# Optimization experiments

Measured on AMD Instinct MI355X. Metric: run time of the kernel, lower is better.

Reference implementation:

```python
import jax, jax.numpy as jnp
import numpy as np

N_NODES = 100000
N_EDGES = 1600000


def _add_self_loops(edge_index, num_nodes):
    loop = jnp.arange(num_nodes, dtype=edge_index.dtype)
    src = jnp.concatenate([edge_index[0], loop])
    dst = jnp.concatenate([edge_index[1], loop])
    return src, dst


def _gcn_conv(x, src, dst, W, b, num_nodes):
    # PyG GCNConv: h = x W, then symmetric-normalized scatter-add aggregation.
    h = x @ W  # [N, F_out]
    ones = jnp.ones(src.shape[0], dtype=x.dtype)
    deg = jax.ops.segment_sum(ones, dst, num_segments=num_nodes)  # in-degree incl. self-loops
    dinv = jnp.where(deg > 0, jax.lax.rsqrt(deg), 0.0)
    norm = dinv[src] * dinv[dst]  # [E]
    msg = h[src] * norm[:, None]  # irregular gather, [E, F_out]
    out = jax.ops.segment_sum(msg, dst, num_segments=num_nodes)  # scatter-add, [N, F_out]
    return out + b


def setup_inputs() -> dict:
    key = jax.random.key(0)
    ks = jax.random.split(key, 4)
    x = jax.random.uniform(ks[0], (N_NODES, 32), dtype=jnp.float32)
    edge_index = jax.random.randint(ks[1], (2, N_EDGES), 0, N_NODES, dtype=jnp.int64)
    W1 = jax.random.normal(ks[2], (32, 64), dtype=jnp.float32) * (1.0 / np.sqrt(32))
    b1 = jnp.zeros((64,), dtype=jnp.float32)
    W2 = jax.random.normal(ks[3], (64, 128), dtype=jnp.float32) * (1.0 / np.sqrt(64))
    b2 = jnp.zeros((128,), dtype=jnp.float32)
    return {"x": x, "edge_index": edge_index, "W1": W1, "b1": b1, "W2": W2, "b2": b2}


def reference(x, edge_index, W1, b1, W2, b2):
    num_nodes = x.shape[0]
    src, dst = _add_self_loops(edge_index, num_nodes)
    h = _gcn_conv(x, src, dst, W1, b1, num_nodes)
    h = jax.nn.relu(h)
    out = _gcn_conv(h, src, dst, W2, b2, num_nodes)
    return out
```

## Files before the change

### kernel.cpp

```cpp
#include <hip/hip_runtime.h>
#include <hip/hip_fp16.h>

static inline int cdiv(int a, int b) { return (a + b - 1) / b; }

#define BK_SHIFT 8
#define NBLK2 1024
#define SCAN_BS 1024
#define MAXB 6144

struct h2x4 { __half2 a, b, c, d; };

__global__ __launch_bounds__(256) void kb1(const int* __restrict__ dst, int E, int epb, int nbuk,
                                           int* __restrict__ cnt) {
    __shared__ int h[512];
    int blk = blockIdx.x;
    for (int b = threadIdx.x; b < nbuk; b += 256) h[b] = 0;
    __syncthreads();
    int beg = blk * epb, end = min(E, beg + epb);
    for (int e = beg + threadIdx.x; e < end; e += 256)
        atomicAdd(&h[dst[e] >> BK_SHIFT], 1);
    __syncthreads();
    for (int b = threadIdx.x; b < nbuk; b += 256) cnt[(size_t)b * NBLK2 + blk] = h[b];
}

__global__ __launch_bounds__(SCAN_BS) void k_blocksum(const int* __restrict__ v, int n, int* __restrict__ bsum) {
    __shared__ int s[SCAN_BS];
    int t = threadIdx.x;
    int i = blockIdx.x * SCAN_BS + t;
    s[t] = (i < n) ? v[i] : 0;
    __syncthreads();
    for (int off = SCAN_BS / 2; off > 0; off >>= 1) {
        if (t < off) s[t] += s[t + off];
        __syncthreads();
    }
    if (t == 0) bsum[blockIdx.x] = s[0];
}

__global__ __launch_bounds__(512) void k_scan_bsums(const int* __restrict__ bsum, int NB, int* __restrict__ boff) {
    __shared__ int s[512];
    int t = threadIdx.x;
    int v = (t < NB) ? bsum[t] : 0;
    s[t] = v;
    __syncthreads();
    for (int off = 1; off < 512; off <<= 1) {
        int u = (t >= off) ? s[t - off] : 0;
        __syncthreads();
        s[t] += u;
        __syncthreads();
    }
    if (t < NB) boff[t] = s[t] - v;
}

__global__ __launch_bounds__(SCAN_BS) void k_scan_final(const int* __restrict__ v, int n,
                                                        const int* __restrict__ boff,
                                                        int* __restrict__ outp, int E) {
    __shared__ int s[SCAN_BS];
    int t = threadIdx.x;
    int i = blockIdx.x * SCAN_BS + t;
    int x = (i < n) ? v[i] : 0;
    s[t] = x;
    __syncthreads();
    for (int off = 1; off < SCAN_BS; off <<= 1) {
        int u = (t >= off) ? s[t - off] : 0;
        __syncthreads();
        s[t] += u;
        __syncthreads();
    }
    if (i < n) outp[i] = boff[blockIdx.x] + s[t] - x;
    if (blockIdx.x == 0 && t == 0) outp[n] = E;
}

__global__ __launch_bounds__(256) void kb2(const int* __restrict__ ei, int E, int epb, int nbuk,
                                           const int* __restrict__ cbase,
                                           unsigned int* __restrict__ pairs) {
    __shared__ int lb[512];
    int blk = blockIdx.x;
    for (int b = threadIdx.x; b < nbuk; b += 256) lb[b] = cbase[(size_t)b * NBLK2 + blk];
    __syncthreads();
    int beg = blk * epb, end = min(E, beg + epb);
    const int* dst = ei + E;
    for (int e = beg + threadIdx.x; e < end; e += 256) {
        int d = dst[e];
        int s = ei[e];
        int slot = atomicAdd(&lb[d >> BK_SHIFT], 1);
        pairs[slot] = (unsigned)s | ((unsigned)(d & 255) << 17);
    }
}

__global__ __launch_bounds__(1024) void k_sortbucket(const unsigned int* __restrict__ pairs,
                                                     const int* __restrict__ cbase, int nbuk, int N, int E,
                                                     int* __restrict__ csr_src,
                                                     int* __restrict__ offsets,
                                                     float* __restrict__ dinv) {
    __shared__ int c[256];
    __shared__ int ex[256];
    __shared__ int sorted[MAXB];
    int b = blockIdx.x;
    int tid = threadIdx.x;
    int base = cbase[(size_t)b * NBLK2];
    int endp = cbase[(size_t)(b + 1) * NBLK2];
    int n = endp - base;
    if (tid < 256) c[tid] = 0;
    __syncthreads();
    int sr_[6], dl_[6], rk_[6];
#pragma unroll
    for (int k = 0; k < 6; ++k) {
        int i = tid + k * 1024;
        if (i < n) {
            unsigned int p = pairs[base + i];
            sr_[k] = (int)(p & 0x1FFFFu);
            dl_[k] = (int)(p >> 17);
            rk_[k] = atomicAdd(&c[dl_[k]], 1);
        }
    }
    __syncthreads();
    if (tid < 256) ex[tid] = c[tid];
    __syncthreads();
    for (int off = 1; off < 256; off <<= 1) {
        int u = (tid >= off && tid < 256) ? ex[tid - off] : 0;
        __syncthreads();
        if (tid < 256) ex[tid] += u;
        __syncthreads();
    }
    if (tid < 256) ex[tid] -= c[tid];
    __syncthreads();
#pragma unroll
    for (int k = 0; k < 6; ++k) {
        int i = tid + k * 1024;
        if (i < n) sorted[ex[dl_[k]] + rk_[k]] = sr_[k];
    }
    __syncthreads();
    for (int i = tid; i < n; i += 1024) csr_src[base + i] = sorted[i];
    if (tid < 256) {
        int g = (b << BK_SHIFT) + tid;
        if (g < N) {
            offsets[g] = base + ex[tid];
            dinv[g] = rsqrtf((float)(c[tid] + 1));
        }
    }
    if (b == 0 && tid == 0) offsets[N] = E;
}

__global__ __launch_bounds__(256) void k_cast32(const float* __restrict__ x, const float* __restrict__ dinv,
                                                __half* __restrict__ xh, int N) {
    int i = blockIdx.x * 256 + threadIdx.x;
    if (i >= N * 8) return;
    int g = i >> 3;
    float di = dinv[g];
    float4 v = ((const float4*)x)[i];
    __half2 h0 = __floats2half2_rn(v.x * di, v.y * di);
    __half2 h1 = __floats2half2_rn(v.z * di, v.w * di);
    ((__half2*)xh)[2 * i] = h0;
    ((__half2*)xh)[2 * i + 1] = h1;
}

template <int F>
__global__ __launch_bounds__(256) void k_agg(const __half* __restrict__ feat,
                                             const int* __restrict__ offsets,
                                             const int* __restrict__ csr_src,
                                             const float* __restrict__ dinv,
                                             float* __restrict__ out, int N) {
    constexpr int L = F / 8;
    int t = blockIdx.x * 256 + threadIdx.x;
    int g = t / L;
    int q = t % L;
    if (g >= N) return;
    const h2x4* f8 = (const h2x4*)feat;
    int beg = offsets[g];
    int end = offsets[g + 1];
    float di = dinv[g];
    float acc[8];
    {
        h2x4 w = f8[(size_t)g * L + q];
        float2 p0 = __half22float2(w.a), p1 = __half22float2(w.b);
        float2 p2 = __half22float2(w.c), p3 = __half22float2(w.d);
        acc[0] = p0.x; acc[1] = p0.y; acc[2] = p1.x; acc[3] = p1.y;
        acc[4] = p2.x; acc[5] = p2.y; acc[6] = p3.x; acc[7] = p3.y;
    }
    int e = beg;
    for (; e + 4 <= end; e += 4) {
        int s0 = csr_src[e + 0], s1 = csr_src[e + 1], s2 = csr_src[e + 2], s3 = csr_src[e + 3];
        h2x4 w0 = f8[(size_t)s0 * L + q];
        h2x4 w1 = f8[(size_t)s1 * L + q];
        h2x4 w2 = f8[(size_t)s2 * L + q];
        h2x4 w3 = f8[(size_t)s3 * L + q];
        float2 u;
        u = __half22float2(w0.a); acc[0] += u.x; acc[1] += u.y;
        u = __half22float2(w0.b); acc[2] += u.x; acc[3] += u.y;
        u = __half22float2(w0.c); acc[4] += u.x; acc[5] += u.y;
        u = __half22float2(w0.d); acc[6] += u.x; acc[7] += u.y;
        u = __half22float2(w1.a); acc[0] += u.x; acc[1] += u.y;
        u = __half22float2(w1.b); acc[2] += u.x; acc[3] += u.y;
        u = __half22float2(w1.c); acc[4] += u.x; acc[5] += u.y;
        u = __half22float2(w1.d); acc[6] += u.x; acc[7] += u.y;
        u = __half22float2(w2.a); acc[0] += u.x; acc[1] += u.y;
        u = __half22float2(w2.b); acc[2] += u.x; acc[3] += u.y;
        u = __half22float2(w2.c); acc[4] += u.x; acc[5] += u.y;
        u = __half22float2(w2.d); acc[6] += u.x; acc[7] += u.y;
        u = __half22float2(w3.a); acc[0] += u.x; acc[1] += u.y;
        u = __half22float2(w3.b); acc[2] += u.x; acc[3] += u.y;
        u = __half22float2(w3.c); acc[4] += u.x; acc[5] += u.y;
        u = __half22float2(w3.d); acc[6] += u.x; acc[7] += u.y;
    }
    for (; e < end; ++e) {
        h2x4 w = f8[(size_t)csr_src[e] * L + q];
        float2 u;
        u = __half22float2(w.a); acc[0] += u.x; acc[1] += u.y;
        u = __half22float2(w.b); acc[2] += u.x; acc[3] += u.y;
        u = __half22float2(w.c); acc[4] += u.x; acc[5] += u.y;
        u = __half22float2(w.d); acc[6] += u.x; acc[7] += u.y;
    }
    float4 o0 = make_float4(acc[0] * di, acc[1] * di, acc[2] * di, acc[3] * di);
    float4 o1 = make_float4(acc[4] * di, acc[5] * di, acc[6] * di, acc[7] * di);
    ((float4*)out)[(size_t)g * (F / 4) + q * 2] = o0;
    ((float4*)out)[(size_t)g * (F / 4) + q * 2 + 1] = o1;
}

__global__ __launch_bounds__(256) void k_gemm1(const float* __restrict__ A, const float* __restrict__ W,
                                               const float* __restrict__ b, const float* __restrict__ dinv,
                                               __half* __restrict__ out, int N) {
    __shared__ float sA[32][68];
    __shared__ float sW[32][64];
    int tid = threadIdx.x;
    int row0 = blockIdx.x * 64;

    {
        const float4* Wv = (const float4*)W;
        float4* sWv = (float4*)&sW[0][0];
        sWv[tid] = Wv[tid];
        sWv[tid + 256] = Wv[tid + 256];
    }
    {
        int row = tid >> 2;
        int gr = row0 + row;
        int kq = (tid & 3) * 4;
#pragma unroll
        for (int i = 0; i < 2; ++i) {
            int k0 = kq + 16 * i;
            float4 v = (gr < N) ? *(const float4*)(A + (size_t)gr * 32 + k0)
                                : make_float4(0.f, 0.f, 0.f, 0.f);
            sA[k0 + 0][row] = v.x;
            sA[k0 + 1][row] = v.y;
            sA[k0 + 2][row] = v.z;
            sA[k0 + 3][row] = v.w;
        }
    }
    __syncthreads();

    int tm = tid & 15, tn = tid >> 4;
    float acc[4][4];
#pragma unroll
    for (int i = 0; i < 4; ++i) {
        float4 bb = *(const float4*)(b + tn * 4);
        acc[i][0] = bb.x; acc[i][1] = bb.y; acc[i][2] = bb.z; acc[i][3] = bb.w;
    }
#pragma unroll 4
    for (int k = 0; k < 32; ++k) {
        float4 a = *(const float4*)&sA[k][tm * 4];
        float4 w = *(const float4*)&sW[k][tn * 4];
        float av[4] = {a.x, a.y, a.z, a.w};
        float wv[4] = {w.x, w.y, w.z, w.w};
#pragma unroll
        for (int i = 0; i < 4; ++i)
#pragma unroll
            for (int j = 0; j < 4; ++j) acc[i][j] = fmaf(av[i], wv[j], acc[i][j]);
    }
#pragma unroll
    for (int i = 0; i < 4; ++i) {
        int row = row0 + tm * 4 + i;
        if (row < N) {
            float di = dinv[row];
            __half2 p0 = __floats2half2_rn(fmaxf(acc[i][0], 0.f) * di, fmaxf(acc[i][1], 0.f) * di);
            __half2 p1 = __floats2half2_rn(fmaxf(acc[i][2], 0.f) * di, fmaxf(acc[i][3], 0.f) * di);
            __half2* op = (__half2*)(out + (size_t)row * 64);
            op[tn * 2] = p0;
            op[tn * 2 + 1] = p1;
        }
    }
}

__global__ __launch_bounds__(256) void k_gemm2(const float* __restrict__ A, const float* __restrict__ W,
                                               const float* __restrict__ b, float* __restrict__ out, int N) {
    __shared__ float sA[64][68];
    __shared__ float sW[64][128];
    int tid = threadIdx.x;
    int row0 = blockIdx.x * 64;

    {
        const float4* Wv = (const float4*)W;
        float4* sWv = (float4*)&sW[0][0];
#pragma unroll
        for (int i = 0; i < 8; ++i) sWv[tid + 256 * i] = Wv[tid + 256 * i];
    }
    {
        int row = tid >> 2;
        int gr = row0 + row;
        int kq = (tid & 3) * 4;
#pragma unroll
        for (int i = 0; i < 4; ++i) {
            int k0 = kq + 16 * i;
            float4 v = (gr < N) ? *(const float4*)(A + (size_t)gr * 64 + k0)
                                : make_float4(0.f, 0.f, 0.f, 0.f);
            sA[k0 + 0][row] = v.x;
            sA[k0 + 1][row] = v.y;
            sA[k0 + 2][row] = v.z;
            sA[k0 + 3][row] = v.w;
        }
    }
    __syncthreads();

    int tm = tid & 15, tn = tid >> 4;
    float acc[4][8];
    {
        float4 b0 = *(const float4*)(b + tn * 8);
        float4 b1 = *(const float4*)(b + tn * 8 + 4);
#pragma unroll
        for (int i = 0; i < 4; ++i) {
            acc[i][0] = b0.x; acc[i][1] = b0.y; acc[i][2] = b0.z; acc[i][3] = b0.w;
            acc[i][4] = b1.x; acc[i][5] = b1.y; acc[i][6] = b1.z; acc[i][7] = b1.w;
        }
    }
#pragma unroll 4
    for (int k = 0; k < 64; ++k) {
        float4 a = *(const float4*)&sA[k][tm * 4];
        float4 w0 = *(const float4*)&sW[k][tn * 8];
        float4 w1 = *(const float4*)&sW[k][tn * 8 + 4];
        float av[4] = {a.x, a.y, a.z, a.w};
        float wv[8] = {w0.x, w0.y, w0.z, w0.w, w1.x, w1.y, w1.z, w1.w};
#pragma unroll
        for (int i = 0; i < 4; ++i)
#pragma unroll
            for (int j = 0; j < 8; ++j) acc[i][j] = fmaf(av[i], wv[j], acc[i][j]);
    }
#pragma unroll
    for (int i = 0; i < 4; ++i) {
        int row = row0 + tm * 4 + i;
        if (row < N) {
            *(float4*)(out + (size_t)row * 128 + tn * 8) =
                make_float4(acc[i][0], acc[i][1], acc[i][2], acc[i][3]);
            *(float4*)(out + (size_t)row * 128 + tn * 8 + 4) =
                make_float4(acc[i][4], acc[i][5], acc[i][6], acc[i][7]);
        }
    }
}

extern "C" void kernel_launch(void* const* d_in, const int* in_sizes, int n_in,
                              void* d_out, int out_size, void* d_ws, size_t ws_size,
                              hipStream_t stream) {
    const float* x  = (const float*)d_in[0];
    const int*   ei = (const int*)d_in[1];
    const float* W1 = (const float*)d_in[2];
    const float* b1 = (const float*)d_in[3];
    const float* W2 = (const float*)d_in[4];
    const float* b2 = (const float*)d_in[5];
    float* out = (float*)d_out;

    const int N = in_sizes[0] / 32;
    const int E = in_sizes[1] / 2;
    const int epb = cdiv(E, NBLK2);
    const int nbuk = cdiv(N, 1 << BK_SHIFT);
    const int clen = nbuk * NBLK2;

    char* ws = (char*)d_ws;
    size_t off = 0;
    auto walloc = [&](size_t bytes) -> void* {
        void* p = ws + off;
        off = (off + bytes + 255) & ~(size_t)255;
        return p;
    };
    int*          cnt     = (int*)          walloc((size_t)(clen + 4) * 4);
    int*          cbase   = (int*)          walloc((size_t)(clen + 4) * 4);
    int*          bsum    = (int*)          walloc(512 * 4);
    int*          boff    = (int*)          walloc(512 * 4);
    unsigned int* pairs   = (unsigned int*) walloc((size_t)E * 4);
    int*          csr_src = (int*)          walloc((size_t)E * 4);
    int*          offsets = (int*)          walloc((size_t)(N + 4) * 4);
    float*        dinv    = (float*)        walloc((size_t)N * 4);
    __half*       xh      = (__half*)       walloc((size_t)N * 32 * 2);
    float*        a1      = (float*)        walloc((size_t)N * 32 * 4);
    __half*       h2h     = (__half*)       walloc((size_t)N * 64 * 2);
    float*        a2      = (float*)        walloc((size_t)N * 64 * 4);
    (void)ws_size; (void)n_in; (void)out_size;

    kb1<<<NBLK2, 256, 0, stream>>>(ei + E, E, epb, nbuk, cnt);

    const int NB = cdiv(clen, SCAN_BS);
    k_blocksum<<<NB, SCAN_BS, 0, stream>>>(cnt, clen, bsum);
    k_scan_bsums<<<1, 512, 0, stream>>>(bsum, NB, boff);
    k_scan_final<<<NB, SCAN_BS, 0, stream>>>(cnt, clen, boff, cbase, E);

    kb2<<<NBLK2, 256, 0, stream>>>(ei, E, epb, nbuk, cbase, pairs);
    k_sortbucket<<<nbuk, 1024, 0, stream>>>(pairs, cbase, nbuk, N, E, csr_src, offsets, dinv);

    k_cast32<<<cdiv(N * 8, 256), 256, 0, stream>>>(x, dinv, xh, N);

    k_agg<32><<<cdiv(N * 4, 256), 256, 0, stream>>>(xh, offsets, csr_src, dinv, a1, N);
    k_gemm1<<<cdiv(N, 64), 256, 0, stream>>>(a1, W1, b1, dinv, h2h, N);

    k_agg<64><<<cdiv(N * 8, 256), 256, 0, stream>>>(h2h, offsets, csr_src, dinv, a2, N);
    k_gemm2<<<cdiv(N, 64), 256, 0, stream>>>(a2, W2, b2, out, N);
}
```

Before: 151.6 us.

## Fuse sparse aggregation with dense GEMM in both GCN layers

Merges each aggregation kernel with the following small GEMM. The aggregated rows now stay in shared memory instead of being written to and re-read from fp32 global buffers a1/a2, and two launches are removed. The second layer's tile shrinks to 32 rows, so each block reloads the full 32KB W2 more often. The gather phase and the GEMM phase also can no longer overlap across separate kernels.

```diff
diff --git a/kernel.cpp b/kernel.cpp
--- a/kernel.cpp
+++ b/kernel.cpp
@@ -154,75 +154,18 @@
     ((__half2*)xh)[2 * i + 1] = h1;
 }
 
-template <int F>
-__global__ __launch_bounds__(256) void k_agg(const __half* __restrict__ feat,
-                                             const int* __restrict__ offsets,
-                                             const int* __restrict__ csr_src,
-                                             const float* __restrict__ dinv,
-                                             float* __restrict__ out, int N) {
-    constexpr int L = F / 8;
-    int t = blockIdx.x * 256 + threadIdx.x;
-    int g = t / L;
-    int q = t % L;
-    if (g >= N) return;
-    const h2x4* f8 = (const h2x4*)feat;
-    int beg = offsets[g];
-    int end = offsets[g + 1];
-    float di = dinv[g];
-    float acc[8];
-    {
-        h2x4 w = f8[(size_t)g * L + q];
-        float2 p0 = __half22float2(w.a), p1 = __half22float2(w.b);
-        float2 p2 = __half22float2(w.c), p3 = __half22float2(w.d);
-        acc[0] = p0.x; acc[1] = p0.y; acc[2] = p1.x; acc[3] = p1.y;
-        acc[4] = p2.x; acc[5] = p2.y; acc[6] = p3.x; acc[7] = p3.y;
-    }
-    int e = beg;
-    for (; e + 4 <= end; e += 4) {
-        int s0 = csr_src[e + 0], s1 = csr_src[e + 1], s2 = csr_src[e + 2], s3 = csr_src[e + 3];
-        h2x4 w0 = f8[(size_t)s0 * L + q];
-        h2x4 w1 = f8[(size_t)s1 * L + q];
-        h2x4 w2 = f8[(size_t)s2 * L + q];
-        h2x4 w3 = f8[(size_t)s3 * L + q];
-        float2 u;
-        u = __half22float2(w0.a); acc[0] += u.x; acc[1] += u.y;
-        u = __half22float2(w0.b); acc[2] += u.x; acc[3] += u.y;
-        u = __half22float2(w0.c); acc[4] += u.x; acc[5] += u.y;
-        u = __half22float2(w0.d); acc[6] += u.x; acc[7] += u.y;
-        u = __half22float2(w1.a); acc[0] += u.x; acc[1] += u.y;
-        u = __half22float2(w1.b); acc[2] += u.x; acc[3] += u.y;
-        u = __half22float2(w1.c); acc[4] += u.x; acc[5] += u.y;
-        u = __half22float2(w1.d); acc[6] += u.x; acc[7] += u.y;
-        u = __half22float2(w2.a); acc[0] += u.x; acc[1] += u.y;
-        u = __half22float2(w2.b); acc[2] += u.x; acc[3] += u.y;
-        u = __half22float2(w2.c); acc[4] += u.x; acc[5] += u.y;
-        u = __half22float2(w2.d); acc[6] += u.x; acc[7] += u.y;
-        u = __half22float2(w3.a); acc[0] += u.x; acc[1] += u.y;
-        u = __half22float2(w3.b); acc[2] += u.x; acc[3] += u.y;
-        u = __half22float2(w3.c); acc[4] += u.x; acc[5] += u.y;
-        u = __half22float2(w3.d); acc[6] += u.x; acc[7] += u.y;
-    }
-    for (; e < end; ++e) {
-        h2x4 w = f8[(size_t)csr_src[e] * L + q];
-        float2 u;
-        u = __half22float2(w.a); acc[0] += u.x; acc[1] += u.y;
-        u = __half22float2(w.b); acc[2] += u.x; acc[3] += u.y;
-        u = __half22float2(w.c); acc[4] += u.x; acc[5] += u.y;
-        u = __half22float2(w.d); acc[6] += u.x; acc[7] += u.y;
-    }
-    float4 o0 = make_float4(acc[0] * di, acc[1] * di, acc[2] * di, acc[3] * di);
-    float4 o1 = make_float4(acc[4] * di, acc[5] * di, acc[6] * di, acc[7] * di);
-    ((float4*)out)[(size_t)g * (F / 4) + q * 2] = o0;
-    ((float4*)out)[(size_t)g * (F / 4) + q * 2 + 1] = o1;
-}
-
-__global__ __launch_bounds__(256) void k_gemm1(const float* __restrict__ A, const float* __restrict__ W,
-                                               const float* __restrict__ b, const float* __restrict__ dinv,
-                                               __half* __restrict__ out, int N) {
-    __shared__ float sA[32][68];
+__global__ __launch_bounds__(256) void k_fused1(const __half* __restrict__ feat,
+                                                const int* __restrict__ offsets,
+                                                const int* __restrict__ csr_src,
+                                                const float* __restrict__ dinv,
+                                                const float* __restrict__ W,
+                                                const float* __restrict__ b,
+                                                __half* __restrict__ out, int N) {
+    __shared__ float sX[64][33];
     __shared__ float sW[32][64];
+    __shared__ float sDi[64];
     int tid = threadIdx.x;
-    int row0 = blockIdx.x * 64;
+    int g0 = blockIdx.x * 64;
 
     {
         const float4* Wv = (const float4*)W;
@@ -231,47 +174,89 @@
         sWv[tid + 256] = Wv[tid + 256];
     }
     {
-        int row = tid >> 2;
-        int gr = row0 + row;
-        int kq = (tid & 3) * 4;
-#pragma unroll
-        for (int i = 0; i < 2; ++i) {
-            int k0 = kq + 16 * i;
-            float4 v = (gr < N) ? *(const float4*)(A + (size_t)gr * 32 + k0)
-                                : make_float4(0.f, 0.f, 0.f, 0.f);
-            sA[k0 + 0][row] = v.x;
-            sA[k0 + 1][row] = v.y;
-            sA[k0 + 2][row] = v.z;
-            sA[k0 + 3][row] = v.w;
-        }
-    }
-    __syncthreads();
-
+        int gl = tid >> 2, q = tid & 3;
+        int g = g0 + gl;
+        const h2x4* f8 = (const h2x4*)feat;
+        float acc[8] = {0.f, 0.f, 0.f, 0.f, 0.f, 0.f, 0.f, 0.f};
+        float di = 0.f;
+        if (g < N) {
+            di = dinv[g];
+            h2x4 w = f8[(size_t)g * 4 + q];
+            float2 u;
+            u = __half22float2(w.a); acc[0] = u.x; acc[1] = u.y;
+            u = __half22float2(w.b); acc[2] = u.x; acc[3] = u.y;
+            u = __half22float2(w.c); acc[4] = u.x; acc[5] = u.y;
+            u = __half22float2(w.d); acc[6] = u.x; acc[7] = u.y;
+            int beg = offsets[g], end = offsets[g + 1];
+            int e = beg;
+            for (; e + 4 <= end; e += 4) {
+                int s0 = csr_src[e + 0], s1 = csr_src[e + 1], s2 = csr_src[e + 2], s3 = csr_src[e + 3];
+                h2x4 w0 = f8[(size_t)s0 * 4 + q];
+                h2x4 w1 = f8[(size_t)s1 * 4 + q];
+                h2x4 w2 = f8[(size_t)s2 * 4 + q];
+                h2x4 w3 = f8[(size_t)s3 * 4 + q];
+                u = __half22float2(w0.a); acc[0] += u.x; acc[1] += u.y;
+                u = __half22float2(w0.b); acc[2] += u.x; acc[3] += u.y;
+                u = __half22float2(w0.c); acc[4] += u.x; acc[5] += u.y;
+                u = __half22float2(w0.d); acc[6] += u.x; acc[7] += u.y;
+                u = __half22float2(w1.a); acc[0] += u.x; acc[1] += u.y;
+                u = __half22float2(w1.b); acc[2] += u.x; acc[3] += u.y;
+                u = __half22float2(w1.c); acc[4] += u.x; acc[5] += u.y;
+                u = __half22float2(w1.d); acc[6] += u.x; acc[7] += u.y;
+                u = __half22float2(w2.a); acc[0] += u.x; acc[1] += u.y;
+                u = __half22float2(w2.b); acc[2] += u.x; acc[3] += u.y;
+                u = __half22float2(w2.c); acc[4] += u.x; acc[5] += u.y;
+                u = __half22float2(w2.d); acc[6] += u.x; acc[7] += u.y;
+                u = __half22float2(w3.a); acc[0] += u.x; acc[1] += u.y;
+                u = __half22float2(w3.b); acc[2] += u.x; acc[3] += u.y;
+                u = __half22float2(w3.c); acc[4] += u.x; acc[5] += u.y;
+                u = __half22float2(w3.d); acc[6] += u.x; acc[7] += u.y;
+            }
+            for (; e < end; ++e) {
+                h2x4 w4 = f8[(size_t)csr_src[e] * 4 + q];
+                u = __half22float2(w4.a); acc[0] += u.x; acc[1] += u.y;
+                u = __half22float2(w4.b); acc[2] += u.x; acc[3] += u.y;
+                u = __half22float2(w4.c); acc[4] += u.x; acc[5] += u.y;
+                u = __half22float2(w4.d); acc[6] += u.x; acc[7] += u.y;
+            }
+        }
+        if (q == 0) sDi[gl] = di;
+#pragma unroll
+        for (int j = 0; j < 8; ++j) sX[gl][q * 8 + j] = acc[j] * di;
+    }
+    __syncthreads();
     int tm = tid & 15, tn = tid >> 4;
-    float acc[4][4];
-#pragma unroll
-    for (int i = 0; i < 4; ++i) {
+    float acc2[4][4];
+    {
         float4 bb = *(const float4*)(b + tn * 4);
-        acc[i][0] = bb.x; acc[i][1] = bb.y; acc[i][2] = bb.z; acc[i][3] = bb.w;
+#pragma unroll
+        for (int i = 0; i < 4; ++i) {
+            acc2[i][0] = bb.x; acc2[i][1] = bb.y; acc2[i][2] = bb.z; acc2[i][3] = bb.w;
+        }
     }
 #pragma unroll 4
     for (int k = 0; k < 32; ++k) {
-        float4 a = *(const float4*)&sA[k][tm * 4];
+        float a0 = sX[tm * 4 + 0][k];
+        float a1 = sX[tm * 4 + 1][k];
+        float a2 = sX[tm * 4 + 2][k];
+        float a3 = sX[tm * 4 + 3][k];
         float4 w = *(const float4*)&sW[k][tn * 4];
-        float av[4] = {a.x, a.y, a.z, a.w};
         float wv[4] = {w.x, w.y, w.z, w.w};
 #pragma unroll
-        for (int i = 0; i < 4; ++i)
-#pragma unroll
-            for (int j = 0; j < 4; ++j) acc[i][j] = fmaf(av[i], wv[j], acc[i][j]);
+        for (int j = 0; j < 4; ++j) {
+            acc2[0][j] = fmaf(a0, wv[j], acc2[0][j]);
+            acc2[1][j] = fmaf(a1, wv[j], acc2[1][j]);
+            acc2[2][j] = fmaf(a2, wv[j], acc2[2][j]);
+            acc2[3][j] = fmaf(a3, wv[j], acc2[3][j]);
+        }
     }
 #pragma unroll
     for (int i = 0; i < 4; ++i) {
-        int row = row0 + tm * 4 + i;
+        int row = g0 + tm * 4 + i;
         if (row < N) {
-            float di = dinv[row];
-            __half2 p0 = __floats2half2_rn(fmaxf(acc[i][0], 0.f) * di, fmaxf(acc[i][1], 0.f) * di);
-            __half2 p1 = __floats2half2_rn(fmaxf(acc[i][2], 0.f) * di, fmaxf(acc[i][3], 0.f) * di);
+            float di = sDi[tm * 4 + i];
+            __half2 p0 = __floats2half2_rn(fmaxf(acc2[i][0], 0.f) * di, fmaxf(acc2[i][1], 0.f) * di);
+            __half2 p1 = __floats2half2_rn(fmaxf(acc2[i][2], 0.f) * di, fmaxf(acc2[i][3], 0.f) * di);
             __half2* op = (__half2*)(out + (size_t)row * 64);
             op[tn * 2] = p0;
             op[tn * 2 + 1] = p1;
@@ -279,12 +264,17 @@
     }
 }
 
-__global__ __launch_bounds__(256) void k_gemm2(const float* __restrict__ A, const float* __restrict__ W,
-                                               const float* __restrict__ b, float* __restrict__ out, int N) {
-    __shared__ float sA[64][68];
+__global__ __launch_bounds__(256) void k_fused2(const __half* __restrict__ feat,
+                                                const int* __restrict__ offsets,
+                                                const int* __restrict__ csr_src,
+                                                const float* __restrict__ dinv,
+                                                const float* __restrict__ W,
+                                                const float* __restrict__ b,
+                                                float* __restrict__ out, int N) {
+    __shared__ float sX[32][69];
     __shared__ float sW[64][128];
     int tid = threadIdx.x;
-    int row0 = blockIdx.x * 64;
+    int g0 = blockIdx.x * 32;
 
     {
         const float4* Wv = (const float4*)W;
@@ -293,53 +283,88 @@
         for (int i = 0; i < 8; ++i) sWv[tid + 256 * i] = Wv[tid + 256 * i];
     }
     {
-        int row = tid >> 2;
-        int gr = row0 + row;
-        int kq = (tid & 3) * 4;
-#pragma unroll
-        for (int i = 0; i < 4; ++i) {
-            int k0 = kq + 16 * i;
-            float4 v = (gr < N) ? *(const float4*)(A + (size_t)gr * 64 + k0)
-                                : make_float4(0.f, 0.f, 0.f, 0.f);
-            sA[k0 + 0][row] = v.x;
-            sA[k0 + 1][row] = v.y;
-            sA[k0 + 2][row] = v.z;
-            sA[k0 + 3][row] = v.w;
-        }
-    }
-    __syncthreads();
-
+        int gl = tid >> 3, q = tid & 7;
+        int g = g0 + gl;
+        const h2x4* f8 = (const h2x4*)feat;
+        float acc[8] = {0.f, 0.f, 0.f, 0.f, 0.f, 0.f, 0.f, 0.f};
+        float di = 0.f;
+        if (g < N) {
+            di = dinv[g];
+            h2x4 w = f8[(size_t)g * 8 + q];
+            float2 u;
+            u = __half22float2(w.a); acc[0] = u.x; acc[1] = u.y;
+            u = __half22float2(w.b); acc[2] = u.x; acc[3] = u.y;
+            u = __half22float2(w.c); acc[4] = u.x; acc[5] = u.y;
+            u = __half22float2(w.d); acc[6] = u.x; acc[7] = u.y;
+            int beg = offsets[g], end = offsets[g + 1];
+            int e = beg;
+            for (; e + 4 <= end; e += 4) {
+                int s0 = csr_src[e + 0], s1 = csr_src[e + 1], s2 = csr_src[e + 2], s3 = csr_src[e + 3];
+                h2x4 w0 = f8[(size_t)s0 * 8 + q];
+                h2x4 w1 = f8[(size_t)s1 * 8 + q];
+                h2x4 w2 = f8[(size_t)s2 * 8 + q];
+                h2x4 w3 = f8[(size_t)s3 * 8 + q];
+                u = __half22float2(w0.a); acc[0] += u.x; acc[1] += u.y;
+                u = __half22float2(w0.b); acc[2] += u.x; acc[3] += u.y;
+                u = __half22float2(w0.c); acc[4] += u.x; acc[5] += u.y;
+                u = __half22float2(w0.d); acc[6] += u.x; acc[7] += u.y;
+                u = __half22float2(w1.a); acc[0] += u.x; acc[1] += u.y;
+                u = __half22float2(w1.b); acc[2] += u.x; acc[3] += u.y;
+                u = __half22float2(w1.c); acc[4] += u.x; acc[5] += u.y;
+                u = __half22float2(w1.d); acc[6] += u.x; acc[7] += u.y;
+                u = __half22float2(w2.a); acc[0] += u.x; acc[1] += u.y;
+                u = __half22float2(w2.b); acc[2] += u.x; acc[3] += u.y;
+                u = __half22float2(w2.c); acc[4] += u.x; acc[5] += u.y;
+                u = __half22float2(w2.d); acc[6] += u.x; acc[7] += u.y;
+                u = __half22float2(w3.a); acc[0] += u.x; acc[1] += u.y;
+                u = __half22float2(w3.b); acc[2] += u.x; acc[3] += u.y;
+                u = __half22float2(w3.c); acc[4] += u.x; acc[5] += u.y;
+                u = __half22float2(w3.d); acc[6] += u.x; acc[7] += u.y;
+            }
+            for (; e < end; ++e) {
+                h2x4 w4 = f8[(size_t)csr_src[e] * 8 + q];
+                u = __half22float2(w4.a); acc[0] += u.x; acc[1] += u.y;
+                u = __half22float2(w4.b); acc[2] += u.x; acc[3] += u.y;
+                u = __half22float2(w4.c); acc[4] += u.x; acc[5] += u.y;
+                u = __half22float2(w4.d); acc[6] += u.x; acc[7] += u.y;
+            }
+        }
+#pragma unroll
+        for (int j = 0; j < 8; ++j) sX[gl][q * 8 + j] = acc[j] * di;
+    }
+    __syncthreads();
     int tm = tid & 15, tn = tid >> 4;
-    float acc[4][8];
+    float acc2[2][8];
     {
         float4 b0 = *(const float4*)(b + tn * 8);
         float4 b1 = *(const float4*)(b + tn * 8 + 4);
 #pragma unroll
-        for (int i = 0; i < 4; ++i) {
-            acc[i][0] = b0.x; acc[i][1] = b0.y; acc[i][2] = b0.z; acc[i][3] = b0.w;
-            acc[i][4] = b1.x; acc[i][5] = b1.y; acc[i][6] = b1.z; acc[i][7] = b1.w;
+        for (int i = 0; i < 2; ++i) {
+            acc2[i][0] = b0.x; acc2[i][1] = b0.y; acc2[i][2] = b0.z; acc2[i][3] = b0.w;
+            acc2[i][4] = b1.x; acc2[i][5] = b1.y; acc2[i][6] = b1.z; acc2[i][7] = b1.w;
         }
     }
 #pragma unroll 4
     for (int k = 0; k < 64; ++k) {
-        float4 a = *(const float4*)&sA[k][tm * 4];
+        float a0 = sX[tm * 2 + 0][k];
+        float a1 = sX[tm * 2 + 1][k];
         float4 w0 = *(const float4*)&sW[k][tn * 8];
         float4 w1 = *(const float4*)&sW[k][tn * 8 + 4];
-        float av[4] = {a.x, a.y, a.z, a.w};
         float wv[8] = {w0.x, w0.y, w0.z, w0.w, w1.x, w1.y, w1.z, w1.w};
 #pragma unroll
-        for (int i = 0; i < 4; ++i)
-#pragma unroll
-            for (int j = 0; j < 8; ++j) acc[i][j] = fmaf(av[i], wv[j], acc[i][j]);
-    }
-#pragma unroll
-    for (int i = 0; i < 4; ++i) {
-        int row = row0 + tm * 4 + i;
+        for (int j = 0; j < 8; ++j) {
+            acc2[0][j] = fmaf(a0, wv[j], acc2[0][j]);
+            acc2[1][j] = fmaf(a1, wv[j], acc2[1][j]);
+        }
+    }
+#pragma unroll
+    for (int i = 0; i < 2; ++i) {
+        int row = g0 + tm * 2 + i;
         if (row < N) {
             *(float4*)(out + (size_t)row * 128 + tn * 8) =
-                make_float4(acc[i][0], acc[i][1], acc[i][2], acc[i][3]);
+                make_float4(acc2[i][0], acc2[i][1], acc2[i][2], acc2[i][3]);
             *(float4*)(out + (size_t)row * 128 + tn * 8 + 4) =
-                make_float4(acc[i][4], acc[i][5], acc[i][6], acc[i][7]);
+                make_float4(acc2[i][4], acc2[i][5], acc2[i][6], acc2[i][7]);
         }
     }
 }
@@ -377,9 +402,7 @@
     int*          offsets = (int*)          walloc((size_t)(N + 4) * 4);
     float*        dinv    = (float*)        walloc((size_t)N * 4);
     __half*       xh      = (__half*)       walloc((size_t)N * 32 * 2);
-    float*        a1      = (float*)        walloc((size_t)N * 32 * 4);
     __half*       h2h     = (__half*)       walloc((size_t)N * 64 * 2);
-    float*        a2      = (float*)        walloc((size_t)N * 64 * 4);
     (void)ws_size; (void)n_in; (void)out_size;
 
     kb1<<<NBLK2, 256, 0, stream>>>(ei + E, E, epb, nbuk, cnt);
@@ -394,9 +417,6 @@
 
     k_cast32<<<cdiv(N * 8, 256), 256, 0, stream>>>(x, dinv, xh, N);
 
-    k_agg<32><<<cdiv(N * 4, 256), 256, 0, stream>>>(xh, offsets, csr_src, dinv, a1, N);
-    k_gemm1<<<cdiv(N, 64), 256, 0, stream>>>(a1, W1, b1, dinv, h2h, N);
-
-    k_agg<64><<<cdiv(N * 8, 256), 256, 0, stream>>>(h2h, offsets, csr_src, dinv, a2, N);
-    k_gemm2<<<cdiv(N, 64), 256, 0, stream>>>(a2, W2, b2, out, N);
-}
+    k_fused1<<<cdiv(N, 64), 256, 0, stream>>>(xh, offsets, csr_src, dinv, W1, b1, h2h, N);
+    k_fused2<<<cdiv(N, 32), 256, 0, stream>>>(h2h, offsets, csr_src, dinv, W2, b2, out, N);
+}
```

Result: faster. 148.2 us (-2.2%).
